# Kernel optimization log

Hardware: AMD Instinct MI355X
Metric: run time of the kernel (lower is better)

## Reference

```python
import jax, jax.numpy as jnp
import numpy as np

ALPHA = 0.2  # LeakyReLU negative slope
NEG_INF = -9e15


def setup_inputs() -> dict:
    key = jax.random.key(0)
    k1, k2, k3, k4, k5 = jax.random.split(key, 5)
    N, F_in, F_out = 8192, 128, 64
    h = jax.random.normal(k1, (N, F_in), dtype=jnp.float32)
    adj = jax.random.randint(k2, (N, N), 0, 2, dtype=jnp.int32)
    edge_feat = jax.random.normal(k3, (N, N), dtype=jnp.float32)
    W = jax.random.normal(k4, (F_in, F_out), dtype=jnp.float32) * 0.1
    a = jax.random.normal(k5, (2 * F_out + 1, 1), dtype=jnp.float32) * 0.1
    return {"h": h, "adj": adj, "edge_feat": edge_feat, "W": W, "a": a}


def reference(h, adj, edge_feat, W, a):
    # Wh: [N, F']
    Wh = h @ W
    F_out = W.shape[1]
    # Decompose the linear score over the concatenated features:
    # e[i,j] = leakyrelu( Wh[i].a1 + Wh[j].a2 + edge_feat[i,j]*a_e )
    a1 = a[:F_out, 0]          # applied to source (row i) features
    a2 = a[F_out:2 * F_out, 0]  # applied to target (col j) features
    a_e = a[2 * F_out, 0]       # applied to scalar edge feature
    s1 = Wh @ a1               # [N]
    s2 = Wh @ a2               # [N]
    e = s1[:, None] + s2[None, :] + edge_feat * a_e  # [N, N]
    e = jnp.where(e > 0, e, ALPHA * e)  # LeakyReLU
    e = jnp.where(adj > 0, e, NEG_INF)
    attention = jax.nn.softmax(e, axis=1)  # [N, N]
    h_prime = attention @ Wh               # [N, F']
    return jax.nn.elu(h_prime)
```

## Files before the change

kernel.cpp:

```cpp
#include <hip/hip_runtime.h>
#include <hip/hip_bf16.h>

#define N_NODES 8192
#define F_IN    128
#define F_OUT   64
#define GAT_ALPHA 0.2f
#define JSPLIT  16
#define COLS_PER_SPLIT (N_NODES / JSPLIT)
#define KSTEPS  (COLS_PER_SPLIT / 32)

typedef short  short8_t  __attribute__((ext_vector_type(8)));
typedef float  f32x4_t   __attribute__((ext_vector_type(4)));

static __device__ __forceinline__ unsigned short f32_to_bf16_bits(float x) {
    unsigned int u = __float_as_uint(x);
    unsigned int r = (u + 0x7fffu + ((u >> 16) & 1u)) >> 16;
    return (unsigned short)r;
}

__global__ __launch_bounds__(256) void k_wh(
    const float* __restrict__ h, const float* __restrict__ W, const float* __restrict__ a,
    unsigned short* __restrict__ wht, float* __restrict__ s1, float* __restrict__ s2)
{
    __shared__ float Wl[F_IN][F_OUT];
    int tid = threadIdx.x;
    #pragma unroll
    for (int i = 0; i < (F_IN * F_OUT) / 256; ++i) {
        int idx = tid + i * 256;
        Wl[idx >> 6][idx & 63] = W[idx];
    }
    __syncthreads();
    int wave = tid >> 6, lane = tid & 63;
    int row = blockIdx.x * 4 + wave;
    const float* hr = h + (size_t)row * F_IN;
    float acc = 0.f;
    #pragma unroll
    for (int k = 0; k < F_IN; k += 4) {
        float4 hv = *(const float4*)(hr + k);
        acc += hv.x * Wl[k + 0][lane];
        acc += hv.y * Wl[k + 1][lane];
        acc += hv.z * Wl[k + 2][lane];
        acc += hv.w * Wl[k + 3][lane];
    }
    wht[(size_t)lane * N_NODES + row] = f32_to_bf16_bits(acc);
    float p1 = acc * a[lane];
    float p2 = acc * a[F_OUT + lane];
    #pragma unroll
    for (int off = 32; off > 0; off >>= 1) {
        p1 += __shfl_down(p1, off);
        p2 += __shfl_down(p2, off);
    }
    if (lane == 0) { s1[row] = p1; s2[row] = p2; }
}

__global__ __launch_bounds__(256) void k_attn(
    const int* __restrict__ adj, const float* __restrict__ ef,
    const float* __restrict__ a,
    const float* __restrict__ s1, const float* __restrict__ s2,
    const unsigned short* __restrict__ wht,
    float* __restrict__ Osum, float* __restrict__ lsum)
{
    int tid  = threadIdx.x;
    int wave = tid >> 6, lane = tid & 63;
    int q = lane >> 4, m = lane & 15;
    int rowtile = blockIdx.x / JSPLIT;
    int split   = blockIdx.x % JSPLIT;
    int row0  = rowtile * 64 + wave * 16;
    int row_m = row0 + m;
    int jbase = split * COLS_PER_SPLIT;

    float s1v = s1[row_m];
    float a_e = a[2 * F_OUT];

    const int*   adjr = adj + (size_t)row_m * N_NODES + jbase;
    const float* efr  = ef  + (size_t)row_m * N_NODES + jbase;
    const float* s2r  = s2 + jbase;
    const unsigned short* wb = wht + jbase;
    const int coff = q * 8;

    f32x4_t acc0 = {0.f, 0.f, 0.f, 0.f};
    f32x4_t acc1 = acc0, acc2 = acc0, acc3 = acc0;
    float lac = 0.f;

    #pragma unroll 2
    for (int kk = 0; kk < KSTEPS; ++kk) {
        int c = kk * 32 + coff;
        int4   aj0 = *(const int4*)(adjr + c);
        int4   aj1 = *(const int4*)(adjr + c + 4);
        float4 ev0 = *(const float4*)(efr + c);
        float4 ev1 = *(const float4*)(efr + c + 4);
        float4 sv0 = *(const float4*)(s2r + c);
        float4 sv1 = *(const float4*)(s2r + c + 4);

        short8_t af;
        float e, p;
        e = fmaf(ev0.x, a_e, s1v + sv0.x); e = fmaxf(e, GAT_ALPHA * e); p = (aj0.x > 0) ? __expf(e) : 0.f; lac += p; af[0] = (short)f32_to_bf16_bits(p);
        e = fmaf(ev0.y, a_e, s1v + sv0.y); e = fmaxf(e, GAT_ALPHA * e); p = (aj0.y > 0) ? __expf(e) : 0.f; lac += p; af[1] = (short)f32_to_bf16_bits(p);
        e = fmaf(ev0.z, a_e, s1v + sv0.z); e = fmaxf(e, GAT_ALPHA * e); p = (aj0.z > 0) ? __expf(e) : 0.f; lac += p; af[2] = (short)f32_to_bf16_bits(p);
        e = fmaf(ev0.w, a_e, s1v + sv0.w); e = fmaxf(e, GAT_ALPHA * e); p = (aj0.w > 0) ? __expf(e) : 0.f; lac += p; af[3] = (short)f32_to_bf16_bits(p);
        e = fmaf(ev1.x, a_e, s1v + sv1.x); e = fmaxf(e, GAT_ALPHA * e); p = (aj1.x > 0) ? __expf(e) : 0.f; lac += p; af[4] = (short)f32_to_bf16_bits(p);
        e = fmaf(ev1.y, a_e, s1v + sv1.y); e = fmaxf(e, GAT_ALPHA * e); p = (aj1.y > 0) ? __expf(e) : 0.f; lac += p; af[5] = (short)f32_to_bf16_bits(p);
        e = fmaf(ev1.z, a_e, s1v + sv1.z); e = fmaxf(e, GAT_ALPHA * e); p = (aj1.z > 0) ? __expf(e) : 0.f; lac += p; af[6] = (short)f32_to_bf16_bits(p);
        e = fmaf(ev1.w, a_e, s1v + sv1.w); e = fmaxf(e, GAT_ALPHA * e); p = (aj1.w > 0) ? __expf(e) : 0.f; lac += p; af[7] = (short)f32_to_bf16_bits(p);

        const unsigned short* wp = wb + c;
        short8_t b0 = *(const short8_t*)(wp + (size_t)( 0 + m) * N_NODES);
        short8_t b1 = *(const short8_t*)(wp + (size_t)(16 + m) * N_NODES);
        short8_t b2 = *(const short8_t*)(wp + (size_t)(32 + m) * N_NODES);
        short8_t b3 = *(const short8_t*)(wp + (size_t)(48 + m) * N_NODES);

        acc0 = __builtin_amdgcn_mfma_f32_16x16x32_bf16(af, b0, acc0, 0, 0, 0);
        acc1 = __builtin_amdgcn_mfma_f32_16x16x32_bf16(af, b1, acc1, 0, 0, 0);
        acc2 = __builtin_amdgcn_mfma_f32_16x16x32_bf16(af, b2, acc2, 0, 0, 0);
        acc3 = __builtin_amdgcn_mfma_f32_16x16x32_bf16(af, b3, acc3, 0, 0, 0);
    }

    lac += __shfl_xor(lac, 16);
    lac += __shfl_xor(lac, 32);
    if (q == 0) atomicAdd(&lsum[row_m], lac);

    #pragma unroll
    for (int r = 0; r < 4; ++r) {
        int orow = row0 + q * 4 + r;
        float* op = Osum + (size_t)orow * F_OUT + m;
        atomicAdd(op +  0, acc0[r]);
        atomicAdd(op + 16, acc1[r]);
        atomicAdd(op + 32, acc2[r]);
        atomicAdd(op + 48, acc3[r]);
    }
}

__global__ __launch_bounds__(256) void k_out(
    const float* __restrict__ Osum, const float* __restrict__ lsum, float* __restrict__ out)
{
    int i = blockIdx.x * 256 + threadIdx.x;
    float v = Osum[i] / lsum[i >> 6];
    out[i] = (v > 0.f) ? v : (__expf(v) - 1.f);
}

extern "C" void kernel_launch(void* const* d_in, const int* in_sizes, int n_in,
                              void* d_out, int out_size, void* d_ws, size_t ws_size,
                              hipStream_t stream)
{
    const float* h   = (const float*)d_in[0];
    const int*   adj = (const int*)d_in[1];
    const float* ef  = (const float*)d_in[2];
    const float* W   = (const float*)d_in[3];
    const float* a   = (const float*)d_in[4];
    float* out = (float*)d_out;

    char* ws = (char*)d_ws;
    unsigned short* wht = (unsigned short*)ws;
    float* s1   = (float*)(ws + (size_t)F_OUT * N_NODES * 2);
    float* s2   = s1 + N_NODES;
    float* Osum = s2 + N_NODES;
    float* lsum = Osum + (size_t)N_NODES * F_OUT;

    hipMemsetAsync(Osum, 0, ((size_t)N_NODES * F_OUT + N_NODES) * sizeof(float), stream);

    k_wh  <<<N_NODES / 4, 256, 0, stream>>>(h, W, a, wht, s1, s2);
    k_attn<<<(N_NODES / 64) * JSPLIT, 256, 0, stream>>>(adj, ef, a, s1, s2, wht, Osum, lsum);
    k_out <<<(N_NODES * F_OUT) / 256, 256, 0, stream>>>(Osum, lsum, out);
}
```

Before: 560.9 us.

## Stage probabilities through LDS with coalesced row loads and MFMA row sums

Rewrites the attention kernel so each block loads 128-column chunks of adj and edge_feat with fully coalesced row-major accesses (32 threads per row), computes the exp weights, and stores them as bf16 into a padded LDS tile. Waves then read MFMA A-fragments from LDS. The row-sum denominator is computed with an extra MFMA against a ones vector instead of scalar accumulation and shuffles. This aims to fix the strided per-lane global reads of the large N×N inputs, at the cost of two barriers per chunk, LDS traffic and a denominator that now sums bf16-rounded weights, which changes the normalization slightly.

```diff
diff --git a/kernel.cpp b/kernel.cpp
--- a/kernel.cpp
+++ b/kernel.cpp
@@ -7,15 +7,16 @@
 #define GAT_ALPHA 0.2f
 #define JSPLIT  16
 #define COLS_PER_SPLIT (N_NODES / JSPLIT)
-#define KSTEPS  (COLS_PER_SPLIT / 32)
+#define KC      128
+#define NCHUNK  (COLS_PER_SPLIT / KC)
+#define LDSTR   136
 
 typedef short  short8_t  __attribute__((ext_vector_type(8)));
 typedef float  f32x4_t   __attribute__((ext_vector_type(4)));
 
-static __device__ __forceinline__ unsigned short f32_to_bf16_bits(float x) {
+static __device__ __forceinline__ unsigned int f32_to_bf16_bits(float x) {
     unsigned int u = __float_as_uint(x);
-    unsigned int r = (u + 0x7fffu + ((u >> 16) & 1u)) >> 16;
-    return (unsigned short)r;
+    return (u + 0x7fffu + ((u >> 16) & 1u)) >> 16;
 }
 
 __global__ __launch_bounds__(256) void k_wh(
@@ -42,7 +43,7 @@
         acc += hv.z * Wl[k + 2][lane];
         acc += hv.w * Wl[k + 3][lane];
     }
-    wht[(size_t)lane * N_NODES + row] = f32_to_bf16_bits(acc);
+    wht[(size_t)lane * N_NODES + row] = (unsigned short)f32_to_bf16_bits(acc);
     float p1 = acc * a[lane];
     float p2 = acc * a[F_OUT + lane];
     #pragma unroll
@@ -53,80 +54,97 @@
     if (lane == 0) { s1[row] = p1; s2[row] = p2; }
 }
 
-__global__ __launch_bounds__(256) void k_attn(
+__global__ __launch_bounds__(256, 4) void k_attn(
     const int* __restrict__ adj, const float* __restrict__ ef,
     const float* __restrict__ a,
     const float* __restrict__ s1, const float* __restrict__ s2,
     const unsigned short* __restrict__ wht,
     float* __restrict__ Osum, float* __restrict__ lsum)
 {
+    __shared__ unsigned short pl[64 * LDSTR];
     int tid  = threadIdx.x;
     int wave = tid >> 6, lane = tid & 63;
     int q = lane >> 4, m = lane & 15;
     int rowtile = blockIdx.x / JSPLIT;
     int split   = blockIdx.x % JSPLIT;
-    int row0  = rowtile * 64 + wave * 16;
-    int row_m = row0 + m;
+    int row0  = rowtile * 64;
     int jbase = split * COLS_PER_SPLIT;
 
-    float s1v = s1[row_m];
+    int ca  = (tid & 31) * 4;
+    int ra0 = tid >> 5;
     float a_e = a[2 * F_OUT];
+    float s1v[8];
+    #pragma unroll
+    for (int i = 0; i < 8; ++i) s1v[i] = s1[row0 + i * 8 + ra0];
 
-    const int*   adjr = adj + (size_t)row_m * N_NODES + jbase;
-    const float* efr  = ef  + (size_t)row_m * N_NODES + jbase;
-    const float* s2r  = s2 + jbase;
-    const unsigned short* wb = wht + jbase;
-    const int coff = q * 8;
+    const unsigned short* wm = wht + (size_t)m * N_NODES + jbase;
 
     f32x4_t acc0 = {0.f, 0.f, 0.f, 0.f};
-    f32x4_t acc1 = acc0, acc2 = acc0, acc3 = acc0;
-    float lac = 0.f;
+    f32x4_t acc1 = acc0, acc2 = acc0, acc3 = acc0, accl = acc0;
+    short8_t ones;
+    #pragma unroll
+    for (int i = 0; i < 8; ++i) ones[i] = (short)0x3F80;
 
-    #pragma unroll 2
-    for (int kk = 0; kk < KSTEPS; ++kk) {
-        int c = kk * 32 + coff;
-        int4   aj0 = *(const int4*)(adjr + c);
-        int4   aj1 = *(const int4*)(adjr + c + 4);
-        float4 ev0 = *(const float4*)(efr + c);
-        float4 ev1 = *(const float4*)(efr + c + 4);
-        float4 sv0 = *(const float4*)(s2r + c);
-        float4 sv1 = *(const float4*)(s2r + c + 4);
-
-        short8_t af;
-        float e, p;
-        e = fmaf(ev0.x, a_e, s1v + sv0.x); e = fmaxf(e, GAT_ALPHA * e); p = (aj0.x > 0) ? __expf(e) : 0.f; lac += p; af[0] = (short)f32_to_bf16_bits(p);
-        e = fmaf(ev0.y, a_e, s1v + sv0.y); e = fmaxf(e, GAT_ALPHA * e); p = (aj0.y > 0) ? __expf(e) : 0.f; lac += p; af[1] = (short)f32_to_bf16_bits(p);
-        e = fmaf(ev0.z, a_e, s1v + sv0.z); e = fmaxf(e, GAT_ALPHA * e); p = (aj0.z > 0) ? __expf(e) : 0.f; lac += p; af[2] = (short)f32_to_bf16_bits(p);
-        e = fmaf(ev0.w, a_e, s1v + sv0.w); e = fmaxf(e, GAT_ALPHA * e); p = (aj0.w > 0) ? __expf(e) : 0.f; lac += p; af[3] = (short)f32_to_bf16_bits(p);
-        e = fmaf(ev1.x, a_e, s1v + sv1.x); e = fmaxf(e, GAT_ALPHA * e); p = (aj1.x > 0) ? __expf(e) : 0.f; lac += p; af[4] = (short)f32_to_bf16_bits(p);
-        e = fmaf(ev1.y, a_e, s1v + sv1.y); e = fmaxf(e, GAT_ALPHA * e); p = (aj1.y > 0) ? __expf(e) : 0.f; lac += p; af[5] = (short)f32_to_bf16_bits(p);
-        e = fmaf(ev1.z, a_e, s1v + sv1.z); e = fmaxf(e, GAT_ALPHA * e); p = (aj1.z > 0) ? __expf(e) : 0.f; lac += p; af[6] = (short)f32_to_bf16_bits(p);
-        e = fmaf(ev1.w, a_e, s1v + sv1.w); e = fmaxf(e, GAT_ALPHA * e); p = (aj1.w > 0) ? __expf(e) : 0.f; lac += p; af[7] = (short)f32_to_bf16_bits(p);
-
-        const unsigned short* wp = wb + c;
-        short8_t b0 = *(const short8_t*)(wp + (size_t)( 0 + m) * N_NODES);
-        short8_t b1 = *(const short8_t*)(wp + (size_t)(16 + m) * N_NODES);
-        short8_t b2 = *(const short8_t*)(wp + (size_t)(32 + m) * N_NODES);
-        short8_t b3 = *(const short8_t*)(wp + (size_t)(48 + m) * N_NODES);
-
-        acc0 = __builtin_amdgcn_mfma_f32_16x16x32_bf16(af, b0, acc0, 0, 0, 0);
-        acc1 = __builtin_amdgcn_mfma_f32_16x16x32_bf16(af, b1, acc1, 0, 0, 0);
-        acc2 = __builtin_amdgcn_mfma_f32_16x16x32_bf16(af, b2, acc2, 0, 0, 0);
-        acc3 = __builtin_amdgcn_mfma_f32_16x16x32_bf16(af, b3, acc3, 0, 0, 0);
+    for (int ch = 0; ch < NCHUNK; ++ch) {
+        int cb = jbase + ch * KC + ca;
+        float4 s2q = *(const float4*)(s2 + cb);
+        int4   aj[8];
+        float4 ev[8];
+        #pragma unroll
+        for (int i = 0; i < 8; ++i) {
+            size_t off = (size_t)(row0 + i * 8 + ra0) * N_NODES + cb;
+            aj[i] = *(const int4*)(adj + off);
+            ev[i] = *(const float4*)(ef + off);
+        }
+        #pragma unroll
+        for (int i = 0; i < 8; ++i) {
+            float b0 = s1v[i] + s2q.x, b1 = s1v[i] + s2q.y;
+            float b2 = s1v[i] + s2q.z, b3 = s1v[i] + s2q.w;
+            float e0 = fmaf(ev[i].x, a_e, b0); e0 = fmaxf(e0, GAT_ALPHA * e0);
+            float e1 = fmaf(ev[i].y, a_e, b1); e1 = fmaxf(e1, GAT_ALPHA * e1);
+            float e2 = fmaf(ev[i].z, a_e, b2); e2 = fmaxf(e2, GAT_ALPHA * e2);
+            float e3 = fmaf(ev[i].w, a_e, b3); e3 = fmaxf(e3, GAT_ALPHA * e3);
+            float p0 = (aj[i].x > 0) ? __expf(e0) : 0.f;
+            float p1 = (aj[i].y > 0) ? __expf(e1) : 0.f;
+            float p2 = (aj[i].z > 0) ? __expf(e2) : 0.f;
+            float p3 = (aj[i].w > 0) ? __expf(e3) : 0.f;
+            uint2 pk;
+            pk.x = f32_to_bf16_bits(p0) | (f32_to_bf16_bits(p1) << 16);
+            pk.y = f32_to_bf16_bits(p2) | (f32_to_bf16_bits(p3) << 16);
+            *(uint2*)&pl[(i * 8 + ra0) * LDSTR + ca] = pk;
+        }
+        __syncthreads();
+        int arow = (wave * 16 + m) * LDSTR;
+        #pragma unroll
+        for (int kk = 0; kk < 4; ++kk) {
+            short8_t af = *(const short8_t*)&pl[arow + kk * 32 + q * 8];
+            const unsigned short* wp = wm + ch * KC + kk * 32 + q * 8;
+            short8_t b0 = *(const short8_t*)(wp);
+            short8_t b1 = *(const short8_t*)(wp + (size_t)16 * N_NODES);
+            short8_t b2 = *(const short8_t*)(wp + (size_t)32 * N_NODES);
+            short8_t b3 = *(const short8_t*)(wp + (size_t)48 * N_NODES);
+            acc0 = __builtin_amdgcn_mfma_f32_16x16x32_bf16(af, b0, acc0, 0, 0, 0);
+            acc1 = __builtin_amdgcn_mfma_f32_16x16x32_bf16(af, b1, acc1, 0, 0, 0);
+            acc2 = __builtin_amdgcn_mfma_f32_16x16x32_bf16(af, b2, acc2, 0, 0, 0);
+            acc3 = __builtin_amdgcn_mfma_f32_16x16x32_bf16(af, b3, acc3, 0, 0, 0);
+            accl = __builtin_amdgcn_mfma_f32_16x16x32_bf16(af, ones, accl, 0, 0, 0);
+        }
+        __syncthreads();
     }
-
-    lac += __shfl_xor(lac, 16);
-    lac += __shfl_xor(lac, 32);
-    if (q == 0) atomicAdd(&lsum[row_m], lac);
 
     #pragma unroll
     for (int r = 0; r < 4; ++r) {
-        int orow = row0 + q * 4 + r;
+        int orow = row0 + wave * 16 + q * 4 + r;
         float* op = Osum + (size_t)orow * F_OUT + m;
         atomicAdd(op +  0, acc0[r]);
         atomicAdd(op + 16, acc1[r]);
         atomicAdd(op + 32, acc2[r]);
         atomicAdd(op + 48, acc3[r]);
+    }
+    if (m == 0) {
+        #pragma unroll
+        for (int r = 0; r < 4; ++r)
+            atomicAdd(&lsum[row0 + wave * 16 + q * 4 + r], accl[r]);
     }
 }
 
```

Measured after the change: 557.6 us. Within noise of the previous version (-0.6%).
